# Optimization experiments

Hardware: AMD Instinct MI355X
Metric: run time of the kernel (lower is better)

The kernel has to match this reference:

```python
import jax, jax.numpy as jnp
import numpy as np

TOP_K = 2


def setup_inputs() -> dict:
    key = jax.random.key(0)
    ks = jax.random.split(key, 10)
    D, F, E = 1024, 4096, 8
    s = 0.02  # realistic init scale, keeps activations stable
    return {
        "x": jax.random.normal(ks[0], (2, 4096, D), dtype=jnp.float32),
        "gate_w": jax.random.normal(ks[1], (E, D), dtype=jnp.float32) * s,
        "w1": jax.random.normal(ks[2], (E, F, D), dtype=jnp.float32) * s,
        "b1": jax.random.normal(ks[3], (E, F), dtype=jnp.float32) * s,
        "w2": jax.random.normal(ks[4], (E, D, F), dtype=jnp.float32) * s,
        "b2": jax.random.normal(ks[5], (E, D), dtype=jnp.float32) * s,
        "sw1": jax.random.normal(ks[6], (F, D), dtype=jnp.float32) * s,
        "sb1": jax.random.normal(ks[7], (F,), dtype=jnp.float32) * s,
        "sw2": jax.random.normal(ks[8], (D, F), dtype=jnp.float32) * s,
        "sb2": jax.random.normal(ks[9], (D,), dtype=jnp.float32) * s,
    }


def _ffn(x, w1, b1, w2, b2):
    # GELU(x @ W1^T + b1) @ W2^T + b2 ; torch F.gelu default = exact (erf)
    h = jax.nn.gelu(x @ w1.T + b1, approximate=False)
    return h @ w2.T + b2


def reference(x, gate_w, w1, b1, w2, b2, sw1, sb1, sw2, sb2):
    B, S, D = x.shape
    E = gate_w.shape[0]
    xt = x.reshape(-1, D)  # [T, D]

    # MoEGate: linear -> softmax -> top-k (weights not renormalized)
    scores = jax.nn.softmax(xt @ gate_w.T, axis=-1)  # [T, E]
    topk_w, topk_idx = jax.lax.top_k(scores, TOP_K)  # [T, K]

    # moe_infer: per-expert FFN, combine with top-k gate weights.
    # Reference form: dense per-expert compute, masked combine (combine sum is
    # permutation-invariant so top-k ordering does not matter).
    out = jnp.zeros_like(xt)
    for e in range(E):
        we = jnp.sum(jnp.where(topk_idx == e, topk_w, 0.0), axis=-1)  # [T]
        out = out + we[:, None] * _ffn(xt, w1[e], b1[e], w2[e], b2[e])

    # shared expert applied to the identity input
    out = out + _ffn(xt, sw1, sb1, sw2, sb2)
    return out.reshape(B, S, D)
```

## Files before the change

kernel.cpp:

```cpp
#include <hip/hip_runtime.h>
#include <hip/hip_bf16.h>

typedef __bf16 bf16_t;
typedef __bf16 bf16x4 __attribute__((ext_vector_type(4)));
typedef __bf16 bf16x8 __attribute__((ext_vector_type(8)));
typedef float  f32x4  __attribute__((ext_vector_type(4)));

static constexpr int TT = 8192;
static constexpr int DD = 1024;
static constexpr int FF = 4096;
static constexpr int NSLOT = 2 * TT;
static constexpr int GATE_BLKS = TT / 4;
static constexpr int CVT_BLKS = 9437184 / 256;
static constexpr int EG2_BLKS = 136 * 8;
static constexpr int SG1_BLKS = 64 * 32;

#define R_COUNTS 0
#define R_OFFSET 8
#define R_TSTART 17
#define R_TOTAL  34
#define R_INTS   40

#define GLL(g, l) __builtin_amdgcn_global_load_lds( \
    (__attribute__((address_space(1))) void*)(g), \
    (__attribute__((address_space(3))) void*)(l), 16, 0, 0)

__device__ __forceinline__ float fast_gelu(float v) {
  float t = -1.5957691216f * v - 0.0713548162f * (v * v * v);
  return v / (1.f + __expf(t));
}

__global__ __launch_bounds__(256) void prep_kernel(const float* __restrict__ x,
                                                   const float* __restrict__ gw,
                                                   float* __restrict__ topkw,
                                                   int* __restrict__ slote,
                                                   bf16_t* __restrict__ xb,
                                                   const float* __restrict__ w1,
                                                   const float* __restrict__ w2,
                                                   const float* __restrict__ sw1,
                                                   const float* __restrict__ sw2,
                                                   bf16_t* __restrict__ wdst) {
  if ((int)blockIdx.x >= GATE_BLKS) {
    size_t i = (size_t)(blockIdx.x - GATE_BLKS) * 256 + threadIdx.x;
    const float* src;
    size_t off;
    if (i < 4194304)      { src = w1;  off = i; }
    else if (i < 8388608) { src = w2;  off = i - 4194304; }
    else if (i < 8912896) { src = sw1; off = i - 8388608; }
    else                  { src = sw2; off = i - 8912896; }
    const float4* s = reinterpret_cast<const float4*>(src) + off * 2;
    float4 a = s[0], b = s[1];
    bf16x8 v;
    v[0] = (bf16_t)a.x; v[1] = (bf16_t)a.y; v[2] = (bf16_t)a.z; v[3] = (bf16_t)a.w;
    v[4] = (bf16_t)b.x; v[5] = (bf16_t)b.y; v[6] = (bf16_t)b.z; v[7] = (bf16_t)b.w;
    *reinterpret_cast<bf16x8*>(wdst + i * 8) = v;
    return;
  }
  int wid = threadIdx.x >> 6, lane = threadIdx.x & 63;
  int t = blockIdx.x * 4 + wid;
  const float4* xv = reinterpret_cast<const float4*>(x + (size_t)t * DD) + lane * 4;
  const float4* gv = reinterpret_cast<const float4*>(gw);
  float acc[8];
  float4 xs[4];
#pragma unroll
  for (int e = 0; e < 8; ++e) acc[e] = 0.f;
#pragma unroll
  for (int i = 0; i < 4; ++i) {
    float4 xi = xv[i];
    xs[i] = xi;
#pragma unroll
    for (int e = 0; e < 8; ++e) {
      float4 g = gv[e * 256 + lane * 4 + i];
      acc[e] += xi.x * g.x + xi.y * g.y + xi.z * g.z + xi.w * g.w;
    }
  }
  {
    bf16x8 lo, hi;
    lo[0]=(bf16_t)xs[0].x; lo[1]=(bf16_t)xs[0].y; lo[2]=(bf16_t)xs[0].z; lo[3]=(bf16_t)xs[0].w;
    lo[4]=(bf16_t)xs[1].x; lo[5]=(bf16_t)xs[1].y; lo[6]=(bf16_t)xs[1].z; lo[7]=(bf16_t)xs[1].w;
    hi[0]=(bf16_t)xs[2].x; hi[1]=(bf16_t)xs[2].y; hi[2]=(bf16_t)xs[2].z; hi[3]=(bf16_t)xs[2].w;
    hi[4]=(bf16_t)xs[3].x; hi[5]=(bf16_t)xs[3].y; hi[6]=(bf16_t)xs[3].z; hi[7]=(bf16_t)xs[3].w;
    bf16_t* d = xb + (size_t)t * DD + lane * 16;
    *reinterpret_cast<bf16x8*>(d) = lo;
    *reinterpret_cast<bf16x8*>(d + 8) = hi;
  }
#pragma unroll
  for (int e = 0; e < 8; ++e)
    for (int off = 32; off; off >>= 1) acc[e] += __shfl_xor(acc[e], off, 64);
  if (lane == 0) {
    float m = acc[0];
#pragma unroll
    for (int e = 1; e < 8; ++e) m = fmaxf(m, acc[e]);
    float p[8], s = 0.f;
#pragma unroll
    for (int e = 0; e < 8; ++e) { p[e] = expf(acc[e] - m); s += p[e]; }
    float inv = 1.f / s;
#pragma unroll
    for (int e = 0; e < 8; ++e) p[e] *= inv;
    int e1 = 0; float b1v = p[0];
#pragma unroll
    for (int e = 1; e < 8; ++e) if (p[e] > b1v) { b1v = p[e]; e1 = e; }
    int e2 = -1; float b2v = -1.f;
#pragma unroll
    for (int e = 0; e < 8; ++e) if (e != e1 && p[e] > b2v) { b2v = p[e]; e2 = e; }
    topkw[2 * t] = b1v;  topkw[2 * t + 1] = b2v;
    slote[2 * t] = e1;   slote[2 * t + 1] = e2;
  }
}

__global__ __launch_bounds__(256) void route_kernel(const int* __restrict__ slote,
                                                    int* __restrict__ routing,
                                                    int* __restrict__ perm,
                                                    int* __restrict__ pos) {
  __shared__ int sl[16384];
  __shared__ int red[256];
  __shared__ int wtot[4];
  const int e = blockIdx.x;
  const int t = threadIdx.x;
  const int lane = t & 63, wid = t >> 6;

  for (int i = t; i < NSLOT; i += 256) sl[i] = slote[i];
  __syncthreads();

  int cnt[8];
#pragma unroll
  for (int ee = 0; ee < 8; ++ee) cnt[ee] = 0;
  for (int i = t; i < NSLOT; i += 256) ++cnt[sl[i]];

  int tot[8];
#pragma unroll
  for (int ee = 0; ee < 8; ++ee) {
    red[t] = cnt[ee];
    __syncthreads();
    for (int s = 128; s; s >>= 1) {
      if (t < s) red[t] += red[t + s];
      __syncthreads();
    }
    tot[ee] = red[0];
    __syncthreads();
  }

  int offarr[9], tstart[9];
  {
    int off = 0, tts = 0;
#pragma unroll
    for (int ee = 0; ee < 8; ++ee) {
      offarr[ee] = off; tstart[ee] = tts;
      off += tot[ee]; tts += (tot[ee] + 127) >> 7;
    }
    offarr[8] = off; tstart[8] = tts;
  }
  if (e == 0 && t == 0) {
#pragma unroll
    for (int ee = 0; ee < 8; ++ee) routing[R_COUNTS + ee] = tot[ee];
#pragma unroll
    for (int ee = 0; ee < 9; ++ee) {
      routing[R_OFFSET + ee] = offarr[ee];
      routing[R_TSTART + ee] = tstart[ee];
    }
    routing[R_TOTAL] = tstart[8];
  }

  int running = offarr[e];
  for (int base = 0; base < NSLOT; base += 256) {
    int s = base + t;
    bool m = (sl[s] == e);
    unsigned long long mask = __ballot(m);
    int wrank = __popcll(mask & ((1ull << lane) - 1ull));
    if (lane == 0) wtot[wid] = __popcll(mask);
    __syncthreads();
    int wpre = 0;
#pragma unroll
    for (int w = 0; w < 4; ++w) if (w < wid) wpre += wtot[w];
    int totb = wtot[0] + wtot[1] + wtot[2] + wtot[3];
    if (m) {
      int pp = running + wpre + wrank;
      perm[pp] = s;
      pos[s] = pp;
    }
    running += totb;
    __syncthreads();
  }
}

template <int MODE>
__device__ __forceinline__ void gemm_body(
    int vbid, int nwg, bf16_t* lds,
    const bf16_t* __restrict__ A, const bf16_t* __restrict__ Bw,
    const float* __restrict__ bias, bf16_t* __restrict__ Hout,
    float* __restrict__ out, const int* __restrict__ routing,
    const int* __restrict__ perm, const float* __restrict__ topkw,
    const int* __restrict__ pos, const bf16_t* __restrict__ slotb) {
  constexpr bool EXPERT = (MODE < 2);
  constexpr int K = (MODE == 0 || MODE == 2) ? 1024 : 4096;
  constexpr int NTOT = (MODE == 0 || MODE == 2) ? 4096 : 1024;
  constexpr int NT = NTOT / 128;
  constexpr int NKT = K / 64;
  constexpr int OUTD = (MODE == 0 || MODE == 2) ? FF : DD;

  const int t = threadIdx.x;
  const int lane = t & 63;
  const int wid = t >> 6;
  const int wm = wid >> 1;
  const int wn = wid & 1;

  const int q = nwg >> 3, r = nwg & 7;
  const int xcd = vbid & 7, bi = vbid >> 3;
  const int swz = (xcd < r ? xcd * (q + 1) : r * (q + 1) + (xcd - r) * q) + bi;
  const int mt = swz / NT;
  const int nt = swz & (NT - 1);

  int row0, valid, eidx = 0;
  if constexpr (EXPERT) {
    if (mt >= routing[R_TOTAL]) return;
    int e = 0;
    while (e < 7 && routing[R_TSTART + e + 1] <= mt) ++e;
    eidx = e;
    int lm = mt - routing[R_TSTART + e];
    row0 = routing[R_OFFSET + e] + lm * 128;
    valid = min(128, routing[R_COUNTS + e] - lm * 128);
  } else {
    row0 = mt * 128;
    valid = 128;
  }

  const bf16_t* Bexp = Bw + (EXPERT ? (size_t)eidx * NTOT * K : 0);
  const float* biasp = bias + (EXPERT ? eidx * NTOT : 0);

  const int sub = t >> 3;
  const int lc = (t & 7) ^ (sub & 7);
  const bf16_t* aS[4];
  const bf16_t* bS[4];
#pragma unroll
  for (int i = 0; i < 4; ++i) {
    int lr = sub + i * 32;
    int gr;
    if constexpr (MODE == 0) {
      gr = perm[row0 + min(lr, valid - 1)] >> 1;
    } else if constexpr (MODE == 1) {
      gr = row0 + min(lr, valid - 1);
    } else {
      gr = row0 + lr;
    }
    aS[i] = A + (size_t)gr * K + lc * 8;
    bS[i] = Bexp + (size_t)(nt * 128 + lr) * K + lc * 8;
  }
  bf16_t* const aD = lds + (sub << 6) + ((t & 7) << 3);
  bf16_t* const bD = aD + 8192;

  const int l15 = lane & 15, lq = lane >> 4;

  f32x4 acc[4][4];
#pragma unroll
  for (int m = 0; m < 4; ++m)
#pragma unroll
    for (int n = 0; n < 4; ++n) acc[m][n] = f32x4{0.f, 0.f, 0.f, 0.f};

  for (int kt = 0; kt < NKT; ++kt) {
    const size_t kof = (size_t)kt * 64;
#pragma unroll
    for (int i = 0; i < 4; ++i) {
      GLL(aS[i] + kof, aD + i * 2048);
      GLL(bS[i] + kof, bD + i * 2048);
    }
    __syncthreads();

#pragma unroll
    for (int kk = 0; kk < 2; ++kk) {
      bf16x8 af[4], bfr[4];
#pragma unroll
      for (int m = 0; m < 4; ++m) {
        int ra = wm * 64 + m * 16 + l15;
        int ph = (kk * 4 + lq) ^ (ra & 7);
        af[m] = *reinterpret_cast<const bf16x8*>(&lds[ra * 64 + ph * 8]);
      }
#pragma unroll
      for (int n = 0; n < 4; ++n) {
        int rb = wn * 64 + n * 16 + l15;
        int ph = (kk * 4 + lq) ^ (rb & 7);
        bfr[n] = *reinterpret_cast<const bf16x8*>(&lds[8192 + rb * 64 + ph * 8]);
      }
      __builtin_amdgcn_s_setprio(1);
#pragma unroll
      for (int m = 0; m < 4; ++m)
#pragma unroll
        for (int n = 0; n < 4; ++n)
          acc[m][n] = __builtin_amdgcn_mfma_f32_16x16x32_bf16(af[m], bfr[n], acc[m][n], 0, 0, 0);
      __builtin_amdgcn_s_setprio(0);
    }
    __syncthreads();
  }

  float bc[4];
#pragma unroll
  for (int n = 0; n < 4; ++n) bc[n] = biasp[nt * 128 + wn * 64 + n * 16 + l15];

  if constexpr (MODE != 3) {
    bf16_t* scr = lds;
#pragma unroll
    for (int h = 0; h < 2; ++h) {
      __syncthreads();
      if (wm == h) {
        float wsl[4][4];
        if constexpr (MODE == 1) {
#pragma unroll
          for (int m = 0; m < 4; ++m)
#pragma unroll
            for (int rr = 0; rr < 4; ++rr) {
              int lr = h * 64 + m * 16 + lq * 4 + rr;
              wsl[m][rr] = topkw[perm[row0 + min(lr, valid - 1)]];
            }
        }
#pragma unroll
        for (int m = 0; m < 4; ++m)
#pragma unroll
          for (int n = 0; n < 4; ++n)
#pragma unroll
            for (int rr = 0; rr < 4; ++rr) {
              float v = acc[m][n][rr] + bc[n];
              float o;
              if constexpr (MODE == 1) o = wsl[m][rr] * v;
              else                     o = fast_gelu(v);
              scr[(m * 16 + lq * 4 + rr) * 128 + wn * 64 + n * 16 + l15] = (bf16_t)o;
            }
      }
      __syncthreads();
#pragma unroll
      for (int i = 0; i < 4; ++i) {
        int c = t + i * 256;
        int rowp = c >> 4, cc = c & 15;
        int lr = h * 64 + rowp;
        if (lr < valid) {
          bf16x8 v8 = *reinterpret_cast<const bf16x8*>(&scr[rowp * 128 + cc * 8]);
          *reinterpret_cast<bf16x8*>(&Hout[(size_t)(row0 + lr) * OUTD + nt * 128 + cc * 8]) = v8;
        }
      }
    }
  } else {
    float* scr = reinterpret_cast<float*>(lds);
#pragma unroll
    for (int h = 0; h < 2; ++h) {
      __syncthreads();
      if (wm == h) {
#pragma unroll
        for (int m = 0; m < 4; ++m)
#pragma unroll
          for (int n = 0; n < 4; ++n)
#pragma unroll
            for (int rr = 0; rr < 4; ++rr)
              scr[(m * 16 + lq * 4 + rr) * 128 + wn * 64 + n * 16 + l15] = acc[m][n][rr] + bc[n];
      }
      __syncthreads();
#pragma unroll
      for (int i = 0; i < 8; ++i) {
        int c = t + i * 256;
        int rowp = c >> 5, cc = c & 31;
        int lr = h * 64 + rowp;
        int gp = row0 + lr;
        int p0 = pos[2 * gp], p1 = pos[2 * gp + 1];
        float4 v4 = *reinterpret_cast<const float4*>(&scr[rowp * 128 + cc * 4]);
        bf16x4 s0 = *reinterpret_cast<const bf16x4*>(&slotb[(size_t)p0 * DD + nt * 128 + cc * 4]);
        bf16x4 s1 = *reinterpret_cast<const bf16x4*>(&slotb[(size_t)p1 * DD + nt * 128 + cc * 4]);
        v4.x += (float)s0[0] + (float)s1[0];
        v4.y += (float)s0[1] + (float)s1[1];
        v4.z += (float)s0[2] + (float)s1[2];
        v4.w += (float)s0[3] + (float)s1[3];
        *reinterpret_cast<float4*>(&out[(size_t)gp * OUTD + nt * 128 + cc * 4]) = v4;
      }
    }
  }
}

template <int MODE>
__global__ __launch_bounds__(256, 4) void gemm_single(
    const bf16_t* __restrict__ A, const bf16_t* __restrict__ Bw,
    const float* __restrict__ bias, bf16_t* __restrict__ Hout,
    float* __restrict__ out, const int* __restrict__ routing,
    const int* __restrict__ perm, const float* __restrict__ topkw,
    const int* __restrict__ pos, const bf16_t* __restrict__ slotb) {
  __shared__ __align__(16) bf16_t lds[16384];
  gemm_body<MODE>(blockIdx.x, gridDim.x, lds, A, Bw, bias, Hout, out,
                  routing, perm, topkw, pos, slotb);
}

__global__ __launch_bounds__(256, 4) void gemm_eg2_sg1(
    const bf16_t* __restrict__ Hexp, const bf16_t* __restrict__ w2b,
    const float* __restrict__ b2, bf16_t* __restrict__ slotb,
    const bf16_t* __restrict__ xb, const bf16_t* __restrict__ sw1b,
    const float* __restrict__ sb1, bf16_t* __restrict__ sHbuf,
    const int* __restrict__ routing, const int* __restrict__ perm,
    const float* __restrict__ topkw) {
  __shared__ __align__(16) bf16_t lds[16384];
  if ((int)blockIdx.x < EG2_BLKS) {
    gemm_body<1>(blockIdx.x, EG2_BLKS, lds, Hexp, w2b, b2, slotb, nullptr,
                 routing, perm, topkw, nullptr, nullptr);
  } else {
    gemm_body<2>(blockIdx.x - EG2_BLKS, SG1_BLKS, lds, xb, sw1b, sb1, sHbuf,
                 nullptr, routing, perm, nullptr, nullptr, nullptr);
  }
}

extern "C" void kernel_launch(void* const* d_in, const int* in_sizes, int n_in,
                              void* d_out, int out_size, void* d_ws, size_t ws_size,
                              hipStream_t stream) {
  const float* x   = (const float*)d_in[0];
  const float* gw  = (const float*)d_in[1];
  const float* w1  = (const float*)d_in[2];
  const float* b1  = (const float*)d_in[3];
  const float* w2  = (const float*)d_in[4];
  const float* b2  = (const float*)d_in[5];
  const float* sw1 = (const float*)d_in[6];
  const float* sb1 = (const float*)d_in[7];
  const float* sw2 = (const float*)d_in[8];
  const float* sb2 = (const float*)d_in[9];
  float* out = (float*)d_out;

  char* ws = (char*)d_ws;
  bf16_t* xb    = (bf16_t*)(ws);
  bf16_t* w1b   = (bf16_t*)(ws + ((size_t)16 << 20));
  bf16_t* w2b   = (bf16_t*)(ws + ((size_t)80 << 20));
  bf16_t* sw1b  = (bf16_t*)(ws + ((size_t)144 << 20));
  bf16_t* sw2b  = (bf16_t*)(ws + ((size_t)152 << 20));
  bf16_t* Hbuf  = (bf16_t*)(ws + ((size_t)160 << 20));
  bf16_t* slotb = (bf16_t*)(ws + ((size_t)16 << 20));
  float*  topkw = (float*)(ws + ((size_t)288 << 20));
  int*    slote = (int*)(ws + ((size_t)288 << 20) + 65536);
  int*    perm  = (int*)(ws + ((size_t)288 << 20) + 2 * 65536);
  int*    pos   = (int*)(ws + ((size_t)288 << 20) + 3 * 65536);
  int*    routing = (int*)(ws + ((size_t)288 << 20) + 4 * 65536);

  const bool bigws = ws_size >= ((size_t)368 << 20);
  bf16_t* sHbuf = bigws ? (bf16_t*)(ws + ((size_t)304 << 20)) : Hbuf;

  prep_kernel<<<GATE_BLKS + CVT_BLKS, 256, 0, stream>>>(x, gw, topkw, slote, xb,
                                                        w1, w2, sw1, sw2, w1b);
  route_kernel<<<8, 256, 0, stream>>>(slote, routing, perm, pos);

  gemm_single<0><<<136 * 32, 256, 0, stream>>>(xb, w1b, b1, Hbuf, nullptr, routing,
                                               perm, nullptr, nullptr, nullptr);
  if (bigws) {
    gemm_eg2_sg1<<<EG2_BLKS + SG1_BLKS, 256, 0, stream>>>(Hbuf, w2b, b2, slotb,
                                                          xb, sw1b, sb1, sHbuf,
                                                          routing, perm, topkw);
  } else {
    gemm_single<1><<<EG2_BLKS, 256, 0, stream>>>(Hbuf, w2b, b2, slotb, nullptr,
                                                 routing, perm, topkw, nullptr, nullptr);
    gemm_single<2><<<SG1_BLKS, 256, 0, stream>>>(xb, sw1b, sb1, Hbuf, nullptr,
                                                 routing, perm, nullptr, nullptr, nullptr);
  }
  gemm_single<3><<<64 * 8, 256, 0, stream>>>(sHbuf, sw2b, sb2, nullptr, out, routing,
                                             perm, nullptr, pos, slotb);
}
```

Before: 632.8 us.

## Split weight conversion and overlap w2/sw2 cast with expert GEMM1

Moves the fp32-to-bf16 conversion of w2 and sw2 out of the prep kernel and into extra blocks appended to the first expert GEMM launch. The prep kernel now converts only w1 and sw1. The memory-bound cast can then run alongside the compute-bound GEMM instead of serially before it. The trade-off is that conversion blocks compete with GEMM blocks for bandwidth and CU slots, and whether the two actually overlap depends on block scheduling order.

```diff
diff --git a/kernel.cpp b/kernel.cpp
--- a/kernel.cpp
+++ b/kernel.cpp
@@ -11,7 +11,13 @@
 static constexpr int FF = 4096;
 static constexpr int NSLOT = 2 * TT;
 static constexpr int GATE_BLKS = TT / 4;
-static constexpr int CVT_BLKS = 9437184 / 256;
+static constexpr int W1_CHUNKS  = 8 * FF * DD / 8;
+static constexpr int SW1_CHUNKS = FF * DD / 8;
+static constexpr int CVT1_BLKS  = (W1_CHUNKS + SW1_CHUNKS) / 256;
+static constexpr int W2_CHUNKS  = 8 * DD * FF / 8;
+static constexpr int SW2_CHUNKS = DD * FF / 8;
+static constexpr int CVT2_BLKS  = (W2_CHUNKS + SW2_CHUNKS) / 256;
+static constexpr int EG1_BLKS = 136 * 32;
 static constexpr int EG2_BLKS = 136 * 8;
 static constexpr int SG1_BLKS = 64 * 32;
 
@@ -28,6 +34,16 @@
 __device__ __forceinline__ float fast_gelu(float v) {
   float t = -1.5957691216f * v - 0.0713548162f * (v * v * v);
   return v / (1.f + __expf(t));
+}
+
+__device__ __forceinline__ void cvt_chunk(const float* __restrict__ src, size_t off,
+                                          bf16_t* __restrict__ dst, size_t dof) {
+  const float4* s = reinterpret_cast<const float4*>(src) + off * 2;
+  float4 a = s[0], b = s[1];
+  bf16x8 v;
+  v[0] = (bf16_t)a.x; v[1] = (bf16_t)a.y; v[2] = (bf16_t)a.z; v[3] = (bf16_t)a.w;
+  v[4] = (bf16_t)b.x; v[5] = (bf16_t)b.y; v[6] = (bf16_t)b.z; v[7] = (bf16_t)b.w;
+  *reinterpret_cast<bf16x8*>(dst + dof * 8) = v;
 }
 
 __global__ __launch_bounds__(256) void prep_kernel(const float* __restrict__ x,
@@ -36,24 +52,13 @@
                                                    int* __restrict__ slote,
                                                    bf16_t* __restrict__ xb,
                                                    const float* __restrict__ w1,
-                                                   const float* __restrict__ w2,
                                                    const float* __restrict__ sw1,
-                                                   const float* __restrict__ sw2,
-                                                   bf16_t* __restrict__ wdst) {
+                                                   bf16_t* __restrict__ w1b,
+                                                   bf16_t* __restrict__ sw1b) {
   if ((int)blockIdx.x >= GATE_BLKS) {
     size_t i = (size_t)(blockIdx.x - GATE_BLKS) * 256 + threadIdx.x;
-    const float* src;
-    size_t off;
-    if (i < 4194304)      { src = w1;  off = i; }
-    else if (i < 8388608) { src = w2;  off = i - 4194304; }
-    else if (i < 8912896) { src = sw1; off = i - 8388608; }
-    else                  { src = sw2; off = i - 8912896; }
-    const float4* s = reinterpret_cast<const float4*>(src) + off * 2;
-    float4 a = s[0], b = s[1];
-    bf16x8 v;
-    v[0] = (bf16_t)a.x; v[1] = (bf16_t)a.y; v[2] = (bf16_t)a.z; v[3] = (bf16_t)a.w;
-    v[4] = (bf16_t)b.x; v[5] = (bf16_t)b.y; v[6] = (bf16_t)b.z; v[7] = (bf16_t)b.w;
-    *reinterpret_cast<bf16x8*>(wdst + i * 8) = v;
+    if (i < W1_CHUNKS) cvt_chunk(w1, i, w1b, i);
+    else               cvt_chunk(sw1, i - W1_CHUNKS, sw1b, i - W1_CHUNKS);
     return;
   }
   int wid = threadIdx.x >> 6, lane = threadIdx.x & 63;
@@ -383,6 +388,23 @@
                   routing, perm, topkw, pos, slotb);
 }
 
+__global__ __launch_bounds__(256, 4) void gemm_eg1_cvt(
+    const bf16_t* __restrict__ xb, const bf16_t* __restrict__ w1b,
+    const float* __restrict__ b1, bf16_t* __restrict__ Hbuf,
+    const int* __restrict__ routing, const int* __restrict__ perm,
+    const float* __restrict__ w2, const float* __restrict__ sw2,
+    bf16_t* __restrict__ w2b, bf16_t* __restrict__ sw2b) {
+  __shared__ __align__(16) bf16_t lds[16384];
+  if ((int)blockIdx.x < EG1_BLKS) {
+    gemm_body<0>(blockIdx.x, EG1_BLKS, lds, xb, w1b, b1, Hbuf, nullptr,
+                 routing, perm, nullptr, nullptr, nullptr);
+  } else {
+    size_t i = (size_t)(blockIdx.x - EG1_BLKS) * 256 + threadIdx.x;
+    if (i < W2_CHUNKS) cvt_chunk(w2, i, w2b, i);
+    else               cvt_chunk(sw2, i - W2_CHUNKS, sw2b, i - W2_CHUNKS);
+  }
+}
+
 __global__ __launch_bounds__(256, 4) void gemm_eg2_sg1(
     const bf16_t* __restrict__ Hexp, const bf16_t* __restrict__ w2b,
     const float* __restrict__ b2, bf16_t* __restrict__ slotb,
@@ -432,12 +454,12 @@
   const bool bigws = ws_size >= ((size_t)368 << 20);
   bf16_t* sHbuf = bigws ? (bf16_t*)(ws + ((size_t)304 << 20)) : Hbuf;
 
-  prep_kernel<<<GATE_BLKS + CVT_BLKS, 256, 0, stream>>>(x, gw, topkw, slote, xb,
-                                                        w1, w2, sw1, sw2, w1b);
+  prep_kernel<<<GATE_BLKS + CVT1_BLKS, 256, 0, stream>>>(x, gw, topkw, slote, xb,
+                                                         w1, sw1, w1b, sw1b);
   route_kernel<<<8, 256, 0, stream>>>(slote, routing, perm, pos);
 
-  gemm_single<0><<<136 * 32, 256, 0, stream>>>(xb, w1b, b1, Hbuf, nullptr, routing,
-                                               perm, nullptr, nullptr, nullptr);
+  gemm_eg1_cvt<<<EG1_BLKS + CVT2_BLKS, 256, 0, stream>>>(xb, w1b, b1, Hbuf, routing,
+                                                         perm, w2, sw2, w2b, sw2b);
   if (bigws) {
     gemm_eg2_sg1<<<EG2_BLKS + SG1_BLKS, 256, 0, stream>>>(Hbuf, w2b, b2, slotb,
                                                           xb, sw1b, sb1, sHbuf,
```

Result: no change. 623.4 us (-1.5%).
